# Kernel optimization log

Measured on AMD Instinct MI355X. Metric: run time of the kernel, lower is better.

The kernel has to match this reference:

```python
import jax, jax.numpy as jnp
import numpy as np

N, F, H = 4096, 512, 64
TEMP = 1.0
EPS = 1e-6


def _lin_init(k, fi, fo):
    s = 1.0 / np.sqrt(fi)
    return jax.random.uniform(k, (fi, fo), jnp.float32, -s, s)


def setup_inputs() -> dict:
    key = jax.random.key(0)
    ks = jax.random.split(key, 8)
    adj = jax.random.uniform(ks[0], (N, N), jnp.float32)
    adj = 0.5 * (adj + adj.T)  # symmetric dense adjacency
    x = jax.random.normal(ks[1], (N, F), jnp.float32)
    return {
        'adj': adj,
        'x': x,
        'Wg': _lin_init(ks[2], F, H), 'bg': jnp.zeros((H,), jnp.float32),
        'Wa1': _lin_init(ks[3], H, H), 'ba1': jnp.zeros((H,), jnp.float32),
        'Wa2': _lin_init(ks[4], H, F), 'ba2': jnp.zeros((F,), jnp.float32),
        'Wx1': _lin_init(ks[5], H, H), 'bx1': jnp.zeros((H,), jnp.float32),
        'Wx2': _lin_init(ks[6], H, F), 'bx2': jnp.zeros((F,), jnp.float32),
    }


def _relaxed_bernoulli_st(probs, noise_logistic, temp):
    # pyro RelaxedBernoulliStraightThrough.rsample(): gumbel-sigmoid + hard round w/ ST grad
    p = jnp.clip(probs, EPS, 1.0 - EPS)
    logits = jnp.log(p) - jnp.log1p(-p)
    soft = jax.nn.sigmoid((logits + noise_logistic) / temp)
    hard = jnp.round(soft)
    return soft + jax.lax.stop_gradient(hard - soft)


def _logistic_noise(k, shape):
    u = jax.random.uniform(k, shape, jnp.float32, EPS, 1.0 - EPS)
    return jnp.log(u) - jnp.log1p(-u)


def reference(adj, x, Wg, bg, Wa1, ba1, Wa2, ba2, Wx1, bx1, Wx2, bx2):
    nkey = jax.random.key(42)
    k1, k2 = jax.random.split(nkey)
    # GCN_Body, 1 layer (dropout is eval no-op): h = relu(A @ (X W) + b)
    h = jax.nn.relu(adj @ (x @ Wg) + bg)            # [N, H]
    # MLPA: Z = Linear(ReLU(Linear(h)))
    Z = jax.nn.relu(h @ Wa1 + ba1) @ Wa2 + ba2      # [N, F]
    adj_logits = Z @ Z.T                            # [N, N]
    edge_probs = jax.nn.sigmoid(adj_logits)
    a = _relaxed_bernoulli_st(edge_probs, _logistic_noise(k1, (N, N)), TEMP)
    a = jnp.triu(a, 1)
    a = a + a.T
    # normalize_adj: fill_diagonal_(1); D^{-1/2} A D^{-1/2} (diag matmuls == row/col scaling)
    i = jnp.arange(N)
    a = a.at[i, i].set(1.0)
    d = a.sum(1) ** -0.5                            # [N]
    adj_norm = d[:, None] * a * d[None, :]
    # MLPX feature mask
    mask_logits = jax.nn.relu(h @ Wx1 + bx1) @ Wx2 + bx2  # [N, F]
    mask_probs = jax.nn.sigmoid(mask_logits)
    mask = _relaxed_bernoulli_st(mask_probs, _logistic_noise(k2, (N, F)), TEMP)
    x_new = x * mask
    return (adj_norm, x_new, adj_logits)
```

## Files before the change

### kernel.cpp

```cpp
#include <hip/hip_runtime.h>
#include <cstdint>
#include <cmath>

#define NN 4096
#define FF 512
#define HH 64
#define KSPLIT 8

typedef unsigned short ushort_t;
typedef short bf16x8 __attribute__((ext_vector_type(8)));
typedef float f32x4 __attribute__((ext_vector_type(4)));

__host__ __device__ __forceinline__ uint32_t rotl32(uint32_t x, int r) {
    return (x << r) | (x >> (32 - r));
}

__host__ __device__ __forceinline__ void threefry2x32(uint32_t ks0, uint32_t ks1,
                                                      uint32_t x0, uint32_t x1,
                                                      uint32_t& o0, uint32_t& o1) {
    uint32_t ks2 = ks0 ^ ks1 ^ 0x1BD11BDAu;
    x0 += ks0; x1 += ks1;
    x0 += x1; x1 = rotl32(x1, 13); x1 ^= x0;
    x0 += x1; x1 = rotl32(x1, 15); x1 ^= x0;
    x0 += x1; x1 = rotl32(x1, 26); x1 ^= x0;
    x0 += x1; x1 = rotl32(x1,  6); x1 ^= x0;
    x0 += ks1; x1 += ks2 + 1u;
    x0 += x1; x1 = rotl32(x1, 17); x1 ^= x0;
    x0 += x1; x1 = rotl32(x1, 29); x1 ^= x0;
    x0 += x1; x1 = rotl32(x1, 16); x1 ^= x0;
    x0 += x1; x1 = rotl32(x1, 24); x1 ^= x0;
    x0 += ks2; x1 += ks0 + 2u;
    x0 += x1; x1 = rotl32(x1, 13); x1 ^= x0;
    x0 += x1; x1 = rotl32(x1, 15); x1 ^= x0;
    x0 += x1; x1 = rotl32(x1, 26); x1 ^= x0;
    x0 += x1; x1 = rotl32(x1,  6); x1 ^= x0;
    x0 += ks0; x1 += ks1 + 3u;
    x0 += x1; x1 = rotl32(x1, 17); x1 ^= x0;
    x0 += x1; x1 = rotl32(x1, 29); x1 ^= x0;
    x0 += x1; x1 = rotl32(x1, 16); x1 ^= x0;
    x0 += x1; x1 = rotl32(x1, 24); x1 ^= x0;
    x0 += ks1; x1 += ks2 + 4u;
    x0 += x1; x1 = rotl32(x1, 13); x1 ^= x0;
    x0 += x1; x1 = rotl32(x1, 15); x1 ^= x0;
    x0 += x1; x1 = rotl32(x1, 26); x1 ^= x0;
    x0 += x1; x1 = rotl32(x1,  6); x1 ^= x0;
    x0 += ks2; x1 += ks0 + 5u;
    o0 = x0; o1 = x1;
}

__device__ __forceinline__ uint32_t jax_bits32(uint32_t k0, uint32_t k1, uint32_t j) {
    uint32_t b0, b1;
    threefry2x32(k0, k1, 0u, j, b0, b1);
    return b0 ^ b1;
}

__device__ __forceinline__ float jax_uniform(uint32_t bits) {
    const float minv = 1e-6f;
    const float maxv = (float)(1.0 - 1e-6);
    const float span = maxv - minv;
    float f = __uint_as_float((bits >> 9) | 0x3f800000u) - 1.0f;
    float u = __fadd_rn(__fmul_rn(f, span), minv);
    return fmaxf(minv, u);
}

__device__ __forceinline__ float hard_sample_f(float l, float u) {
    float thr = 1.0f / (1.0f + expf(l));
    return (u > thr) ? 1.0f : 0.0f;
}

__device__ __forceinline__ ushort_t f32_to_bf16_rne(float f) {
    uint32_t x = __float_as_uint(f);
    uint32_t r = (x + 0x7fffu + ((x >> 16) & 1u)) >> 16;
    return (ushort_t)r;
}


__global__ void k_xw(const float* __restrict__ x, const float* __restrict__ Wg,
                     float* __restrict__ T) {
    int col = threadIdx.x;
    int row = blockIdx.x * 4 + threadIdx.y;
    const float* xr = x + row * FF;
    float acc = 0.0f;
    #pragma unroll 4
    for (int k = 0; k < FF; ++k)
        acc += xr[k] * Wg[k * HH + col];
    T[row * HH + col] = acc;
}

__global__ void __launch_bounds__(256)
k_adjT2(const float* __restrict__ adj, const float* __restrict__ T,
        float* __restrict__ partial) {
    __shared__ __align__(16) float As[64][68];
    __shared__ __align__(16) float Ts[64][64];
    int t = threadIdx.x;
    int tx = t & 15, ty = t >> 4;
    int r0 = blockIdx.x * 64;
    int kb = blockIdx.y * (NN / KSPLIT);
    float acc[4][4] = {};
    for (int k0 = 0; k0 < NN / KSPLIT; k0 += 64) {
        __syncthreads();
        for (int n = t; n < 1024; n += 256) {
            int rr = n >> 4, kq = n & 15;
            float4 v = *(const float4*)&adj[(size_t)(r0 + rr) * NN + kb + k0 + kq * 4];
            *(float4*)&As[rr][kq * 4] = v;
        }
        for (int n = t; n < 1024; n += 256) {
            int rr = n >> 4, kq = n & 15;
            float4 v = *(const float4*)&T[(size_t)(kb + k0 + rr) * HH + kq * 4];
            *(float4*)&Ts[rr][kq * 4] = v;
        }
        __syncthreads();
        for (int kk = 0; kk < 64; ++kk) {
            float a[4];
            #pragma unroll
            for (int i = 0; i < 4; ++i) a[i] = As[ty * 4 + i][kk];
            float4 bv = *(float4*)&Ts[kk][tx * 4];
            float b[4] = {bv.x, bv.y, bv.z, bv.w};
            #pragma unroll
            for (int i = 0; i < 4; ++i)
                #pragma unroll
                for (int j = 0; j < 4; ++j)
                    acc[i][j] += a[i] * b[j];
        }
    }
    float* P = partial + (size_t)blockIdx.y * NN * HH;
    #pragma unroll
    for (int i = 0; i < 4; ++i) {
        int row = r0 + ty * 4 + i;
        float4 v = {acc[i][0], acc[i][1], acc[i][2], acc[i][3]};
        *(float4*)&P[(size_t)row * HH + tx * 4] = v;
    }
}

__global__ void k_hred(const float* __restrict__ partial, const float* __restrict__ bg,
                       float* __restrict__ h) {
    int idx = blockIdx.x * 256 + threadIdx.x;
    float s = 0.0f;
    #pragma unroll
    for (int p = 0; p < KSPLIT; ++p) s += partial[(size_t)p * NN * HH + idx];
    float v = s + bg[idx & (HH - 1)];
    h[idx] = v > 0.0f ? v : 0.0f;
}

__global__ void k_small64(const float* __restrict__ A, const float* __restrict__ W,
                          const float* __restrict__ b, float* __restrict__ O) {
    __shared__ float Wl[HH][HH];
    int tx = threadIdx.x, ty = threadIdx.y;
    int tid = ty * 64 + tx;
    for (int n = tid; n < HH * HH; n += 256)
        ((float*)Wl)[n] = W[n];
    __syncthreads();
    int row = blockIdx.x * 4 + ty;
    const float* Ar = A + row * HH;
    float acc = 0.0f;
    #pragma unroll
    for (int k = 0; k < HH; ++k) acc += Ar[k] * Wl[k][tx];
    float v = acc + b[tx];
    O[row * HH + tx] = v > 0.0f ? v : 0.0f;
}

__global__ void k_projZ(const float* __restrict__ A, const float* __restrict__ W,
                        const float* __restrict__ b, ushort_t* __restrict__ Zb) {
    int tx = threadIdx.x, ty = threadIdx.y;
    int row = blockIdx.y * 4 + ty;
    int col = blockIdx.x * 64 + tx;
    const float* Ar = A + row * HH;
    float acc = 0.0f;
    #pragma unroll
    for (int k = 0; k < HH; ++k) acc += Ar[k] * W[k * FF + col];
    Zb[(size_t)row * FF + col] = f32_to_bf16_rne(acc + b[col]);
}

__global__ void k_mask(const float* __restrict__ M1, const float* __restrict__ W,
                       const float* __restrict__ b, const float* __restrict__ x,
                       float* __restrict__ xnew, uint32_t k20, uint32_t k21,
                       float Lmin, float Lmax) {
    int tx = threadIdx.x, ty = threadIdx.y;
    int row = blockIdx.y * 4 + ty;
    int col = blockIdx.x * 64 + tx;
    const float* Ar = M1 + row * HH;
    float acc = 0.0f;
    #pragma unroll
    for (int k = 0; k < HH; ++k) acc += Ar[k] * W[k * FF + col];
    float ml = acc + b[col];
    float l = ml < Lmin ? Lmin : (ml > Lmax ? Lmax : ml);
    uint32_t idx = (uint32_t)row * FF + (uint32_t)col;
    float u = jax_uniform(jax_bits32(k20, k21, idx));
    float m = hard_sample_f(l, u);
    xnew[idx] = (m != 0.0f) ? x[idx] : 0.0f;
}

__global__ void __launch_bounds__(256)
k_zzt_gemm_tri(const ushort_t* __restrict__ Zb, float* __restrict__ out2) {
    __shared__ __align__(16) union {
        struct { ushort_t At[128][72]; ushort_t Bt[128][72]; } s;
        float Tls[32][132];
    } sm;
    int t = threadIdx.x;
    int lane = t & 63, w = t >> 6;
    int lr = lane & 15, lk = lane >> 4;
    int b = blockIdx.x, bi = 0;
    while (b >= 32 - bi) { b -= 32 - bi; ++bi; }
    int bj = bi + b;
    int rbase = bi * 128, cbase = bj * 128;
    f32x4 acc[2][8] = {};
    for (int k0 = 0; k0 < FF; k0 += 64) {
        __syncthreads();
        for (int n = t; n < 1024; n += 256) {
            int rr = n >> 3, ck = n & 7;
            *(uint4*)&sm.s.At[rr][ck * 8] = *(const uint4*)&Zb[(size_t)(rbase + rr) * FF + k0 + ck * 8];
            *(uint4*)&sm.s.Bt[rr][ck * 8] = *(const uint4*)&Zb[(size_t)(cbase + rr) * FF + k0 + ck * 8];
        }
        __syncthreads();
        #pragma unroll
        for (int ks = 0; ks < 2; ++ks) {
            bf16x8 a0 = *(const bf16x8*)&sm.s.At[w * 32 + lr][ks * 32 + lk * 8];
            bf16x8 a1 = *(const bf16x8*)&sm.s.At[w * 32 + 16 + lr][ks * 32 + lk * 8];
            #pragma unroll
            for (int j = 0; j < 8; ++j) {
                bf16x8 bb = *(const bf16x8*)&sm.s.Bt[j * 16 + lr][ks * 32 + lk * 8];
                acc[0][j] = __builtin_amdgcn_mfma_f32_16x16x32_bf16(a0, bb, acc[0][j], 0, 0, 0);
                acc[1][j] = __builtin_amdgcn_mfma_f32_16x16x32_bf16(a1, bb, acc[1][j], 0, 0, 0);
            }
        }
    }
    #pragma unroll
    for (int it = 0; it < 2; ++it) {
        int rg = rbase + w * 32 + it * 16 + lk * 4;
        #pragma unroll
        for (int reg = 0; reg < 4; ++reg)
            #pragma unroll
            for (int j = 0; j < 8; ++j)
                out2[(size_t)(rg + reg) * NN + cbase + j * 16 + lr] = acc[it][j][reg];
    }
    if (bi != bj) {
        #pragma unroll
        for (int g = 0; g < 4; ++g) {
            __syncthreads();
            #pragma unroll
            for (int it = 0; it < 2; ++it)
                #pragma unroll
                for (int jp = 0; jp < 2; ++jp)
                    #pragma unroll
                    for (int reg = 0; reg < 4; ++reg)
                        sm.Tls[jp * 16 + lr][w * 32 + it * 16 + lk * 4 + reg] =
                            acc[it][g * 2 + jp][reg];
            __syncthreads();
            #pragma unroll
            for (int r4 = 0; r4 < 4; ++r4) {
                int tr = r4 * 8 + (t >> 5);
                int tc = (t & 31) * 4;
                float4 v = *(const float4*)&sm.Tls[tr][tc];
                *(float4*)&out2[(size_t)(cbase + g * 32 + tr) * NN + rbase + tc] = v;
            }
        }
    }
}

__global__ void __launch_bounds__(256)
k_sample_tri(const float* __restrict__ out2, uint32_t* __restrict__ mask,
             float* __restrict__ rowsum, uint32_t k10, uint32_t k11,
             float Lmin, float Lmax) {
    __shared__ uint32_t Wl[128][5];
    __shared__ int rs[128], cs[128];
    int t = threadIdx.x;
    int b = blockIdx.x, bi = 0;
    while (b >= 32 - bi) { b -= 32 - bi; ++bi; }
    int bj = bi + b;
    int rbase = bi * 128, cbase = bj * 128;
    if (t < 128) { rs[t] = 0; cs[t] = 0; }
    __syncthreads();
    int rr = t >> 1;
    int r = rbase + rr;
    int rowacc = 0;
    #pragma unroll
    for (int wi = 0; wi < 2; ++wi) {
        int wc = (t & 1) * 2 + wi;
        const float* zr = out2 + (size_t)r * NN + cbase + wc * 32;
        uint32_t word = 0;
        #pragma unroll
        for (int q = 0; q < 8; ++q) {
            float4 zv = *(const float4*)&zr[q * 4];
            float za[4] = {zv.x, zv.y, zv.z, zv.w};
            #pragma unroll
            for (int e4 = 0; e4 < 4; ++e4) {
                int e = q * 4 + e4;
                int c = cbase + wc * 32 + e;
                float z = za[e4];
                float l = z < Lmin ? Lmin : (z > Lmax ? Lmax : z);
                int lo = r < c ? r : c;
                int hi = r < c ? c : r;
                uint32_t idx = (uint32_t)lo * NN + (uint32_t)hi;
                float u = jax_uniform(jax_bits32(k10, k11, idx));
                float thr = 1.0f / (1.0f + expf(l));
                uint32_t bit = (r == c) ? 1u : (u > thr ? 1u : 0u);
                word |= bit << e;
            }
        }
        Wl[rr][wc] = word;
        mask[(size_t)r * (NN / 32) + ((cbase >> 5) + wc)] = word;
        rowacc += __popc(word);
    }
    atomicAdd(&rs[rr], rowacc);
    __syncthreads();
    if (bi != bj) {
        int cc = t >> 1;
        int colacc = 0;
        #pragma unroll
        for (int wi = 0; wi < 2; ++wi) {
            int wr = (t & 1) * 2 + wi;
            uint32_t tw = 0;
            #pragma unroll
            for (int bb = 0; bb < 32; ++bb)
                tw |= ((Wl[wr * 32 + bb][cc >> 5] >> (cc & 31)) & 1u) << bb;
            mask[(size_t)(cbase + cc) * (NN / 32) + ((rbase >> 5) + wr)] = tw;
            colacc += __popc(tw);
        }
        atomicAdd(&cs[cc], colacc);
    }
    __syncthreads();
    if (t < 128) {
        atomicAdd(&rowsum[rbase + t], (float)rs[t]);
        if (bi != bj) atomicAdd(&rowsum[cbase + t], (float)cs[t]);
    }
}

__global__ void k_deg(const float* __restrict__ rowsum, float* __restrict__ dvec) {
    int i = blockIdx.x * 256 + threadIdx.x;
    dvec[i] = 1.0f / sqrtf(rowsum[i]);
}

__global__ void k_scale2(const uint32_t* __restrict__ mask,
                         const float* __restrict__ dvec, float* __restrict__ out0) {
    size_t idx = ((size_t)blockIdx.x * 256 + threadIdx.x) * 4;
    int r = (int)(idx >> 12);
    int c = (int)(idx & 4095);
    uint32_t wv = mask[idx >> 5];
    int sh = (int)(idx & 31);
    float dr = dvec[r];
    float4 dc = *(const float4*)&dvec[c];
    float4 o;
    o.x = ((wv >> (sh + 0)) & 1u) ? dr * dc.x : 0.0f;
    o.y = ((wv >> (sh + 1)) & 1u) ? dr * dc.y : 0.0f;
    o.z = ((wv >> (sh + 2)) & 1u) ? dr * dc.z : 0.0f;
    o.w = ((wv >> (sh + 3)) & 1u) ? dr * dc.w : 0.0f;
    *(float4*)&out0[idx] = o;
}

extern "C" void kernel_launch(void* const* d_in, const int* in_sizes, int n_in,
                              void* d_out, int out_size, void* d_ws, size_t ws_size,
                              hipStream_t stream) {
    const float* adj = (const float*)d_in[0];
    const float* x   = (const float*)d_in[1];
    const float* Wg  = (const float*)d_in[2];
    const float* bg  = (const float*)d_in[3];
    const float* Wa1 = (const float*)d_in[4];
    const float* ba1 = (const float*)d_in[5];
    const float* Wa2 = (const float*)d_in[6];
    const float* ba2 = (const float*)d_in[7];
    const float* Wx1 = (const float*)d_in[8];
    const float* bx1 = (const float*)d_in[9];
    const float* Wx2 = (const float*)d_in[10];
    const float* bx2 = (const float*)d_in[11];

    float* out0 = (float*)d_out;
    float* out1 = out0 + (size_t)NN * NN;
    float* out2 = out1 + (size_t)NN * FF;

    float* T       = (float*)d_ws;
    float* h       = T + NN * HH;
    float* A1      = h + NN * HH;
    float* M1      = A1 + NN * HH;
    ushort_t* Zb   = (ushort_t*)(M1 + NN * HH);
    float* partial = (float*)(Zb + (size_t)NN * FF);
    float* dvec    = partial + (size_t)KSPLIT * NN * HH;
    float* rowsum  = dvec + NN;
    uint32_t* mask = (uint32_t*)partial;

    uint32_t k1a, k1b, k2a, k2b;
    threefry2x32(0u, 42u, 0u, 0u, k1a, k1b);
    threefry2x32(0u, 42u, 0u, 1u, k2a, k2b);

    const float Lmax = (float)(std::log(1.0 - 1e-6) - std::log1p(-(1.0 - 1e-6)));
    const float Lmin = (float)(std::log(1e-6) - std::log1p(-1e-6));

    k_xw<<<NN / 4, dim3(64, 4), 0, stream>>>(x, Wg, T);
    k_adjT2<<<dim3(64, KSPLIT), 256, 0, stream>>>(adj, T, partial);
    k_hred<<<NN * HH / 256, 256, 0, stream>>>(partial, bg, h);
    k_small64<<<NN / 4, dim3(64, 4), 0, stream>>>(h, Wa1, ba1, A1);
    k_projZ<<<dim3(FF / 64, NN / 4), dim3(64, 4), 0, stream>>>(A1, Wa2, ba2, Zb);

    k_zzt_gemm_tri<<<528, 256, 0, stream>>>(Zb, out2);

    hipMemsetAsync(rowsum, 0, NN * sizeof(float), stream);
    k_sample_tri<<<528, 256, 0, stream>>>(out2, mask, rowsum, k1a, k1b, Lmin, Lmax);
    k_deg<<<NN / 256, 256, 0, stream>>>(rowsum, dvec);
    k_scale2<<<NN * NN / 4 / 256, 256, 0, stream>>>(mask, dvec, out0);

    k_small64<<<NN / 4, dim3(64, 4), 0, stream>>>(h, Wx1, bx1, M1);
    k_mask<<<dim3(FF / 64, NN / 4), dim3(64, 4), 0, stream>>>(M1, Wx2, bx2, x, out1,
                                                              k2a, k2b, Lmin, Lmax);
}
```

Before: 443.0 us.

## Use bf16 MFMA for adj@T, fuse MLP stages, widen sampling, inline degree

The A@(XW) product now converts adj tiles to bf16 and runs on MFMA 16x16x32 instructions, reading a transposed bf16 copy of XW written by k_xw. The two-layer MLPs for Z and for the feature mask are each fused into a single kernel, which drops the intermediate A1/M1 buffers and extra launches. The triangular sampling kernel uses 512 threads so each thread handles one mask word. The degree kernel is folded into the final scaling kernel. Rounding adj to bf16 lowers the precision of h, and the fused MLPs may use many registers.

```diff
diff --git a/kernel.cpp b/kernel.cpp
--- a/kernel.cpp
+++ b/kernel.cpp
@@ -76,60 +76,74 @@
 
 
 __global__ void k_xw(const float* __restrict__ x, const float* __restrict__ Wg,
-                     float* __restrict__ T) {
-    int col = threadIdx.x;
-    int row = blockIdx.x * 4 + threadIdx.y;
+                     ushort_t* __restrict__ Tt) {
+    __shared__ ushort_t Tls[4][64];
+    int col = threadIdx.x, ty = threadIdx.y;
+    int row = blockIdx.x * 4 + ty;
     const float* xr = x + row * FF;
     float acc = 0.0f;
     #pragma unroll 4
     for (int k = 0; k < FF; ++k)
         acc += xr[k] * Wg[k * HH + col];
-    T[row * HH + col] = acc;
+    Tls[ty][col] = f32_to_bf16_rne(acc);
+    __syncthreads();
+    int t = ty * 64 + col;
+    if (t < 64) {
+        uint2 v;
+        ushort_t* p = (ushort_t*)&v;
+        p[0] = Tls[0][t]; p[1] = Tls[1][t]; p[2] = Tls[2][t]; p[3] = Tls[3][t];
+        *(uint2*)&Tt[(size_t)t * NN + blockIdx.x * 4] = v;
+    }
 }
 
 __global__ void __launch_bounds__(256)
-k_adjT2(const float* __restrict__ adj, const float* __restrict__ T,
-        float* __restrict__ partial) {
-    __shared__ __align__(16) float As[64][68];
-    __shared__ __align__(16) float Ts[64][64];
+k_adjT_mfma(const float* __restrict__ adj, const ushort_t* __restrict__ Tt,
+            float* __restrict__ partial) {
+    __shared__ __align__(16) ushort_t As[64][72];
+    __shared__ __align__(16) ushort_t Tl[64][72];
     int t = threadIdx.x;
-    int tx = t & 15, ty = t >> 4;
+    int lane = t & 63, w = t >> 6;
+    int lr = lane & 15, lk = lane >> 4;
     int r0 = blockIdx.x * 64;
     int kb = blockIdx.y * (NN / KSPLIT);
-    float acc[4][4] = {};
+    f32x4 acc[4] = {};
     for (int k0 = 0; k0 < NN / KSPLIT; k0 += 64) {
         __syncthreads();
-        for (int n = t; n < 1024; n += 256) {
-            int rr = n >> 4, kq = n & 15;
-            float4 v = *(const float4*)&adj[(size_t)(r0 + rr) * NN + kb + k0 + kq * 4];
-            *(float4*)&As[rr][kq * 4] = v;
-        }
-        for (int n = t; n < 1024; n += 256) {
-            int rr = n >> 4, kq = n & 15;
-            float4 v = *(const float4*)&T[(size_t)(kb + k0 + rr) * HH + kq * 4];
-            *(float4*)&Ts[rr][kq * 4] = v;
+        #pragma unroll
+        for (int i = 0; i < 4; ++i) {
+            int idx = t + i * 256;
+            int rr = idx >> 4;
+            int kq = (idx & 15) * 4;
+            float4 v = *(const float4*)&adj[(size_t)(r0 + rr) * NN + kb + k0 + kq];
+            uint32_t lo = (uint32_t)f32_to_bf16_rne(v.x) | ((uint32_t)f32_to_bf16_rne(v.y) << 16);
+            uint32_t hi = (uint32_t)f32_to_bf16_rne(v.z) | ((uint32_t)f32_to_bf16_rne(v.w) << 16);
+            uint2 pk = {lo, hi};
+            *(uint2*)&As[rr][kq] = pk;
+        }
+        #pragma unroll
+        for (int i = 0; i < 2; ++i) {
+            int idx = t + i * 256;
+            int cc = idx >> 3;
+            int kq = (idx & 7) * 8;
+            *(uint4*)&Tl[cc][kq] = *(const uint4*)&Tt[(size_t)cc * NN + kb + k0 + kq];
         }
         __syncthreads();
-        for (int kk = 0; kk < 64; ++kk) {
-            float a[4];
-            #pragma unroll
-            for (int i = 0; i < 4; ++i) a[i] = As[ty * 4 + i][kk];
-            float4 bv = *(float4*)&Ts[kk][tx * 4];
-            float b[4] = {bv.x, bv.y, bv.z, bv.w};
-            #pragma unroll
-            for (int i = 0; i < 4; ++i)
-                #pragma unroll
-                for (int j = 0; j < 4; ++j)
-                    acc[i][j] += a[i] * b[j];
+        #pragma unroll
+        for (int ks = 0; ks < 2; ++ks) {
+            bf16x8 a = *(const bf16x8*)&As[w * 16 + lr][ks * 32 + lk * 8];
+            #pragma unroll
+            for (int c = 0; c < 4; ++c) {
+                bf16x8 bb = *(const bf16x8*)&Tl[c * 16 + lr][ks * 32 + lk * 8];
+                acc[c] = __builtin_amdgcn_mfma_f32_16x16x32_bf16(a, bb, acc[c], 0, 0, 0);
+            }
         }
     }
     float* P = partial + (size_t)blockIdx.y * NN * HH;
     #pragma unroll
-    for (int i = 0; i < 4; ++i) {
-        int row = r0 + ty * 4 + i;
-        float4 v = {acc[i][0], acc[i][1], acc[i][2], acc[i][3]};
-        *(float4*)&P[(size_t)row * HH + tx * 4] = v;
-    }
+    for (int c = 0; c < 4; ++c)
+        #pragma unroll
+        for (int reg = 0; reg < 4; ++reg)
+            P[(size_t)(r0 + w * 16 + lk * 4 + reg) * HH + c * 16 + lr] = acc[c][reg];
 }
 
 __global__ void k_hred(const float* __restrict__ partial, const float* __restrict__ bg,
@@ -142,52 +156,96 @@
     h[idx] = v > 0.0f ? v : 0.0f;
 }
 
-__global__ void k_small64(const float* __restrict__ A, const float* __restrict__ W,
-                          const float* __restrict__ b, float* __restrict__ O) {
-    __shared__ float Wl[HH][HH];
-    int tx = threadIdx.x, ty = threadIdx.y;
-    int tid = ty * 64 + tx;
-    for (int n = tid; n < HH * HH; n += 256)
-        ((float*)Wl)[n] = W[n];
-    __syncthreads();
-    int row = blockIdx.x * 4 + ty;
-    const float* Ar = A + row * HH;
-    float acc = 0.0f;
-    #pragma unroll
-    for (int k = 0; k < HH; ++k) acc += Ar[k] * Wl[k][tx];
-    float v = acc + b[tx];
-    O[row * HH + tx] = v > 0.0f ? v : 0.0f;
-}
-
-__global__ void k_projZ(const float* __restrict__ A, const float* __restrict__ W,
-                        const float* __restrict__ b, ushort_t* __restrict__ Zb) {
-    int tx = threadIdx.x, ty = threadIdx.y;
-    int row = blockIdx.y * 4 + ty;
-    int col = blockIdx.x * 64 + tx;
-    const float* Ar = A + row * HH;
-    float acc = 0.0f;
-    #pragma unroll
-    for (int k = 0; k < HH; ++k) acc += Ar[k] * W[k * FF + col];
-    Zb[(size_t)row * FF + col] = f32_to_bf16_rne(acc + b[col]);
-}
-
-__global__ void k_mask(const float* __restrict__ M1, const float* __restrict__ W,
-                       const float* __restrict__ b, const float* __restrict__ x,
-                       float* __restrict__ xnew, uint32_t k20, uint32_t k21,
-                       float Lmin, float Lmax) {
-    int tx = threadIdx.x, ty = threadIdx.y;
-    int row = blockIdx.y * 4 + ty;
-    int col = blockIdx.x * 64 + tx;
-    const float* Ar = M1 + row * HH;
-    float acc = 0.0f;
-    #pragma unroll
-    for (int k = 0; k < HH; ++k) acc += Ar[k] * W[k * FF + col];
-    float ml = acc + b[col];
-    float l = ml < Lmin ? Lmin : (ml > Lmax ? Lmax : ml);
-    uint32_t idx = (uint32_t)row * FF + (uint32_t)col;
-    float u = jax_uniform(jax_bits32(k20, k21, idx));
-    float m = hard_sample_f(l, u);
-    xnew[idx] = (m != 0.0f) ? x[idx] : 0.0f;
+__global__ void __launch_bounds__(256)
+k_mlpZ(const float* __restrict__ h, const float* __restrict__ W1,
+       const float* __restrict__ b1, const float* __restrict__ W2,
+       const float* __restrict__ b2, ushort_t* __restrict__ Zb) {
+    __shared__ float W1l[HH][HH];
+    __shared__ float A1l[8][HH];
+    __shared__ float hl[8][HH];
+    int t = threadIdx.x;
+    int r0 = blockIdx.x * 8;
+    for (int n = t; n < HH * HH; n += 256) ((float*)W1l)[n] = W1[n];
+    for (int n = t; n < 8 * HH; n += 256) ((float*)hl)[n] = h[r0 * HH + n];
+    __syncthreads();
+    {
+        int col = t & 63;
+        int rb = t >> 6;
+        #pragma unroll
+        for (int rr = 0; rr < 2; ++rr) {
+            int row = rb * 2 + rr;
+            float acc = b1[col];
+            #pragma unroll
+            for (int k = 0; k < HH; ++k) acc += hl[row][k] * W1l[k][col];
+            A1l[row][col] = acc > 0.0f ? acc : 0.0f;
+        }
+    }
+    __syncthreads();
+    #pragma unroll
+    for (int p = 0; p < 2; ++p) {
+        int col = p * 256 + t;
+        float wc[HH];
+        #pragma unroll
+        for (int k = 0; k < HH; ++k) wc[k] = W2[k * FF + col];
+        float bb = b2[col];
+        #pragma unroll
+        for (int row = 0; row < 8; ++row) {
+            float acc = bb;
+            #pragma unroll
+            for (int k = 0; k < HH; ++k) acc += A1l[row][k] * wc[k];
+            Zb[(size_t)(r0 + row) * FF + col] = f32_to_bf16_rne(acc);
+        }
+    }
+}
+
+__global__ void __launch_bounds__(256)
+k_mlpM(const float* __restrict__ h, const float* __restrict__ W1,
+       const float* __restrict__ b1, const float* __restrict__ W2,
+       const float* __restrict__ b2, const float* __restrict__ x,
+       float* __restrict__ xnew, uint32_t k20, uint32_t k21,
+       float Lmin, float Lmax) {
+    __shared__ float W1l[HH][HH];
+    __shared__ float A1l[8][HH];
+    __shared__ float hl[8][HH];
+    int t = threadIdx.x;
+    int r0 = blockIdx.x * 8;
+    for (int n = t; n < HH * HH; n += 256) ((float*)W1l)[n] = W1[n];
+    for (int n = t; n < 8 * HH; n += 256) ((float*)hl)[n] = h[r0 * HH + n];
+    __syncthreads();
+    {
+        int col = t & 63;
+        int rb = t >> 6;
+        #pragma unroll
+        for (int rr = 0; rr < 2; ++rr) {
+            int row = rb * 2 + rr;
+            float acc = b1[col];
+            #pragma unroll
+            for (int k = 0; k < HH; ++k) acc += hl[row][k] * W1l[k][col];
+            A1l[row][col] = acc > 0.0f ? acc : 0.0f;
+        }
+    }
+    __syncthreads();
+    #pragma unroll
+    for (int p = 0; p < 2; ++p) {
+        int col = p * 256 + t;
+        float wc[HH];
+        #pragma unroll
+        for (int k = 0; k < HH; ++k) wc[k] = W2[k * FF + col];
+        float bb = b2[col];
+        #pragma unroll
+        for (int row = 0; row < 8; ++row) {
+            float acc = bb;
+            #pragma unroll
+            for (int k = 0; k < HH; ++k) acc += A1l[row][k] * wc[k];
+            float ml = acc;
+            float l = ml < Lmin ? Lmin : (ml > Lmax ? Lmax : ml);
+            uint32_t idx = (uint32_t)(r0 + row) * FF + (uint32_t)col;
+            float u = jax_uniform(jax_bits32(k20, k21, idx));
+            float m = hard_sample_f(l, u);
+            size_t gi = (size_t)(r0 + row) * FF + col;
+            xnew[gi] = (m != 0.0f) ? x[gi] : 0.0f;
+        }
+    }
 }
 
 __global__ void __launch_bounds__(256)
@@ -257,7 +315,7 @@
     }
 }
 
-__global__ void __launch_bounds__(256)
+__global__ void __launch_bounds__(512)
 k_sample_tri(const float* __restrict__ out2, uint32_t* __restrict__ mask,
              float* __restrict__ rowsum, uint32_t k10, uint32_t k11,
              float Lmin, float Lmax) {
@@ -270,53 +328,41 @@
     int rbase = bi * 128, cbase = bj * 128;
     if (t < 128) { rs[t] = 0; cs[t] = 0; }
     __syncthreads();
-    int rr = t >> 1;
+    int rr = t >> 2, wc = t & 3;
     int r = rbase + rr;
-    int rowacc = 0;
-    #pragma unroll
-    for (int wi = 0; wi < 2; ++wi) {
-        int wc = (t & 1) * 2 + wi;
-        const float* zr = out2 + (size_t)r * NN + cbase + wc * 32;
-        uint32_t word = 0;
-        #pragma unroll
-        for (int q = 0; q < 8; ++q) {
-            float4 zv = *(const float4*)&zr[q * 4];
-            float za[4] = {zv.x, zv.y, zv.z, zv.w};
-            #pragma unroll
-            for (int e4 = 0; e4 < 4; ++e4) {
-                int e = q * 4 + e4;
-                int c = cbase + wc * 32 + e;
-                float z = za[e4];
-                float l = z < Lmin ? Lmin : (z > Lmax ? Lmax : z);
-                int lo = r < c ? r : c;
-                int hi = r < c ? c : r;
-                uint32_t idx = (uint32_t)lo * NN + (uint32_t)hi;
-                float u = jax_uniform(jax_bits32(k10, k11, idx));
-                float thr = 1.0f / (1.0f + expf(l));
-                uint32_t bit = (r == c) ? 1u : (u > thr ? 1u : 0u);
-                word |= bit << e;
-            }
-        }
-        Wl[rr][wc] = word;
-        mask[(size_t)r * (NN / 32) + ((cbase >> 5) + wc)] = word;
-        rowacc += __popc(word);
-    }
-    atomicAdd(&rs[rr], rowacc);
+    const float* zr = out2 + (size_t)r * NN + cbase + wc * 32;
+    uint32_t word = 0;
+    #pragma unroll
+    for (int q = 0; q < 8; ++q) {
+        float4 zv = *(const float4*)&zr[q * 4];
+        float za[4] = {zv.x, zv.y, zv.z, zv.w};
+        #pragma unroll
+        for (int e4 = 0; e4 < 4; ++e4) {
+            int e = q * 4 + e4;
+            int c = cbase + wc * 32 + e;
+            float z = za[e4];
+            float l = z < Lmin ? Lmin : (z > Lmax ? Lmax : z);
+            int lo = r < c ? r : c;
+            int hi = r < c ? c : r;
+            uint32_t idx = (uint32_t)lo * NN + (uint32_t)hi;
+            float u = jax_uniform(jax_bits32(k10, k11, idx));
+            float thr = 1.0f / (1.0f + expf(l));
+            uint32_t bit = (r == c) ? 1u : (u > thr ? 1u : 0u);
+            word |= bit << e;
+        }
+    }
+    Wl[rr][wc] = word;
+    mask[(size_t)r * (NN / 32) + ((cbase >> 5) + wc)] = word;
+    atomicAdd(&rs[rr], (int)__popc(word));
     __syncthreads();
     if (bi != bj) {
-        int cc = t >> 1;
-        int colacc = 0;
-        #pragma unroll
-        for (int wi = 0; wi < 2; ++wi) {
-            int wr = (t & 1) * 2 + wi;
-            uint32_t tw = 0;
-            #pragma unroll
-            for (int bb = 0; bb < 32; ++bb)
-                tw |= ((Wl[wr * 32 + bb][cc >> 5] >> (cc & 31)) & 1u) << bb;
-            mask[(size_t)(cbase + cc) * (NN / 32) + ((rbase >> 5) + wr)] = tw;
-            colacc += __popc(tw);
-        }
-        atomicAdd(&cs[cc], colacc);
+        int cc = t >> 2, wr = t & 3;
+        uint32_t tw = 0;
+        #pragma unroll
+        for (int bb = 0; bb < 32; ++bb)
+            tw |= ((Wl[wr * 32 + bb][cc >> 5] >> (cc & 31)) & 1u) << bb;
+        mask[(size_t)(cbase + cc) * (NN / 32) + ((rbase >> 5) + wr)] = tw;
+        atomicAdd(&cs[cc], (int)__popc(tw));
     }
     __syncthreads();
     if (t < 128) {
@@ -325,25 +371,20 @@
     }
 }
 
-__global__ void k_deg(const float* __restrict__ rowsum, float* __restrict__ dvec) {
-    int i = blockIdx.x * 256 + threadIdx.x;
-    dvec[i] = 1.0f / sqrtf(rowsum[i]);
-}
-
-__global__ void k_scale2(const uint32_t* __restrict__ mask,
-                         const float* __restrict__ dvec, float* __restrict__ out0) {
+__global__ void k_scale3(const uint32_t* __restrict__ mask,
+                         const float* __restrict__ rowsum, float* __restrict__ out0) {
     size_t idx = ((size_t)blockIdx.x * 256 + threadIdx.x) * 4;
     int r = (int)(idx >> 12);
     int c = (int)(idx & 4095);
     uint32_t wv = mask[idx >> 5];
     int sh = (int)(idx & 31);
-    float dr = dvec[r];
-    float4 dc = *(const float4*)&dvec[c];
+    float dr = 1.0f / sqrtf(rowsum[r]);
+    float4 rc = *(const float4*)&rowsum[c];
     float4 o;
-    o.x = ((wv >> (sh + 0)) & 1u) ? dr * dc.x : 0.0f;
-    o.y = ((wv >> (sh + 1)) & 1u) ? dr * dc.y : 0.0f;
-    o.z = ((wv >> (sh + 2)) & 1u) ? dr * dc.z : 0.0f;
-    o.w = ((wv >> (sh + 3)) & 1u) ? dr * dc.w : 0.0f;
+    o.x = ((wv >> (sh + 0)) & 1u) ? dr * (1.0f / sqrtf(rc.x)) : 0.0f;
+    o.y = ((wv >> (sh + 1)) & 1u) ? dr * (1.0f / sqrtf(rc.y)) : 0.0f;
+    o.z = ((wv >> (sh + 2)) & 1u) ? dr * (1.0f / sqrtf(rc.z)) : 0.0f;
+    o.w = ((wv >> (sh + 3)) & 1u) ? dr * (1.0f / sqrtf(rc.w)) : 0.0f;
     *(float4*)&out0[idx] = o;
 }
 
@@ -367,14 +408,11 @@
     float* out1 = out0 + (size_t)NN * NN;
     float* out2 = out1 + (size_t)NN * FF;
 
-    float* T       = (float*)d_ws;
-    float* h       = T + NN * HH;
-    float* A1      = h + NN * HH;
-    float* M1      = A1 + NN * HH;
-    ushort_t* Zb   = (ushort_t*)(M1 + NN * HH);
-    float* partial = (float*)(Zb + (size_t)NN * FF);
-    float* dvec    = partial + (size_t)KSPLIT * NN * HH;
-    float* rowsum  = dvec + NN;
+    ushort_t* Tt   = (ushort_t*)d_ws;
+    float* h       = (float*)((char*)d_ws + (1 << 20));
+    ushort_t* Zb   = (ushort_t*)(h + NN * HH);
+    float* partial = (float*)((char*)Zb + (size_t)NN * FF * 2);
+    float* rowsum  = partial + (size_t)KSPLIT * NN * HH;
     uint32_t* mask = (uint32_t*)partial;
 
     uint32_t k1a, k1b, k2a, k2b;
@@ -384,20 +422,17 @@
     const float Lmax = (float)(std::log(1.0 - 1e-6) - std::log1p(-(1.0 - 1e-6)));
     const float Lmin = (float)(std::log(1e-6) - std::log1p(-1e-6));
 
-    k_xw<<<NN / 4, dim3(64, 4), 0, stream>>>(x, Wg, T);
-    k_adjT2<<<dim3(64, KSPLIT), 256, 0, stream>>>(adj, T, partial);
+    k_xw<<<NN / 4, dim3(64, 4), 0, stream>>>(x, Wg, Tt);
+    k_adjT_mfma<<<dim3(64, KSPLIT), 256, 0, stream>>>(adj, Tt, partial);
     k_hred<<<NN * HH / 256, 256, 0, stream>>>(partial, bg, h);
-    k_small64<<<NN / 4, dim3(64, 4), 0, stream>>>(h, Wa1, ba1, A1);
-    k_projZ<<<dim3(FF / 64, NN / 4), dim3(64, 4), 0, stream>>>(A1, Wa2, ba2, Zb);
+    k_mlpZ<<<NN / 8, 256, 0, stream>>>(h, Wa1, ba1, Wa2, ba2, Zb);
 
     k_zzt_gemm_tri<<<528, 256, 0, stream>>>(Zb, out2);
 
     hipMemsetAsync(rowsum, 0, NN * sizeof(float), stream);
-    k_sample_tri<<<528, 256, 0, stream>>>(out2, mask, rowsum, k1a, k1b, Lmin, Lmax);
-    k_deg<<<NN / 256, 256, 0, stream>>>(rowsum, dvec);
-    k_scale2<<<NN * NN / 4 / 256, 256, 0, stream>>>(mask, dvec, out0);
-
-    k_small64<<<NN / 4, dim3(64, 4), 0, stream>>>(h, Wx1, bx1, M1);
-    k_mask<<<dim3(FF / 64, NN / 4), dim3(64, 4), 0, stream>>>(M1, Wx2, bx2, x, out1,
-                                                              k2a, k2b, Lmin, Lmax);
-}
+    k_sample_tri<<<528, 512, 0, stream>>>(out2, mask, rowsum, k1a, k1b, Lmin, Lmax);
+    k_scale3<<<NN * NN / 4 / 256, 256, 0, stream>>>(mask, rowsum, out0);
+
+    k_mlpM<<<NN / 8, 256, 0, stream>>>(h, Wx1, bx1, Wx2, bx2, x, out1,
+                                       k2a, k2b, Lmin, Lmax);
+}
```

Result: faster. 393.9 us (-11.1%).
